# Kernel tuning notes

Hardware: AMD Instinct MI355X
Metric: run time of the kernel (lower is better)

## Reference

```python
import jax, jax.numpy as jnp
import numpy as np

N_EMBD = 1024
N_HEAD = 16
BLOCK_SIZE = 2048


def setup_inputs() -> dict:
    key = jax.random.key(0)
    k1, k2, k3 = jax.random.split(key, 3)
    B, T, C = 2, 2048, N_EMBD
    x = jax.random.normal(k1, (B, T, C), dtype=jnp.float32)
    # Dense(3*n_embd, use_bias=False): kernel [C, 3C]
    Wqkv = jax.random.normal(k2, (C, 3 * C), dtype=jnp.float32) * (1.0 / np.sqrt(C))
    # Output Dense(n_embd): kernel [C, C] + bias [C]
    Wout = jax.random.normal(k3, (C, C), dtype=jnp.float32) * (1.0 / np.sqrt(C))
    bout = jnp.zeros((C,), dtype=jnp.float32)
    return {"x": x, "Wqkv": Wqkv, "Wout": Wout, "bout": bout}


def reference(x, Wqkv, Wout, bout):
    B, T, C = x.shape
    H = N_HEAD
    hs = C // H  # head_size

    qkv = x @ Wqkv                       # [B, T, 3C]
    q, k, v = jnp.split(qkv, 3, axis=-1)  # each [B, T, C]
    q = q.reshape(B, T, H, hs).transpose(0, 2, 1, 3)  # [B, H, T, hs]
    k = k.reshape(B, T, H, hs).transpose(0, 2, 1, 3)
    v = v.reshape(B, T, H, hs).transpose(0, 2, 1, 3)

    att = jnp.einsum("bhqd,bhkd->bhqk", q, k) * (hs ** -0.5)  # [B, H, T, T]
    T_use = min(T, BLOCK_SIZE)
    mask = jnp.tril(jnp.ones((T_use, T_use), dtype=bool))
    att = jnp.where(mask, att, -jnp.inf)
    att = jax.nn.softmax(att, axis=-1)
    # dropout: deterministic (training=False) -> identity

    out = jnp.einsum("bhqk,bhkd->bhqd", att, v)  # [B, H, T, hs]
    out = out.transpose(0, 2, 1, 3).reshape(B, T, C)
    out = out @ Wout + bout
    return out
```

## Files before the change

kernel.cpp:

```cpp
#include <hip/hip_runtime.h>
#include <cstdint>
#include <cstddef>

#define BB 2
#define TT 2048
#define CC 1024
#define HH 16
#define HS 64
#define MM (BB*TT)
#define N1 (3*CC)

#define PST2 40

#define QSCALE 0.1803368801111243f

typedef __bf16 bf16_t;
typedef bf16_t bf16x8 __attribute__((ext_vector_type(8)));
typedef float  floatx4 __attribute__((ext_vector_type(4)));

__device__ __forceinline__ bf16_t f2bf(float f) {
    uint32_t u = __builtin_bit_cast(uint32_t, f);
    u += 0x7FFFu + ((u >> 16) & 1u);
    unsigned short s = (unsigned short)(u >> 16);
    return __builtin_bit_cast(bf16_t, s);
}

__device__ __forceinline__ void load_lds16(const bf16_t* g, bf16_t* l) {
    __builtin_amdgcn_global_load_lds((__attribute__((address_space(1))) void*)g,
                                     (__attribute__((address_space(3))) void*)l,
                                     16, 0, 0);
}

__device__ __forceinline__ void transpose_body(const float* __restrict__ src,
                                               bf16_t* __restrict__ dst,
                                               int R, int Ccol, int bx, int by,
                                               int tx, int ty, bf16_t (*tile)[33]) {
    int c0 = bx * 32, r0 = by * 32;
    for (int i = ty; i < 32; i += 8)
        tile[i][tx] = f2bf(src[(size_t)(r0 + i) * Ccol + c0 + tx]);
    __syncthreads();
    for (int i = ty; i < 32; i += 8)
        dst[(size_t)(c0 + i) * R + r0 + tx] = tile[tx][i];
}

__global__ __launch_bounds__(256) void k_prep(const float* __restrict__ x,
                                              const float* __restrict__ Wqkv,
                                              const float* __restrict__ Wout,
                                              bf16_t* __restrict__ xb,
                                              bf16_t* __restrict__ Wt1,
                                              bf16_t* __restrict__ Wt2) {
    __shared__ bf16_t tile[32][33];
    const int bid = blockIdx.x, tid = threadIdx.x;
    if (bid < 2048) {
        size_t i = ((size_t)bid * 256 + tid) * 8;
        float4 a = *(const float4*)(x + i);
        float4 b = *(const float4*)(x + i + 4);
        bf16x8 o;
        o[0] = f2bf(a.x); o[1] = f2bf(a.y); o[2] = f2bf(a.z); o[3] = f2bf(a.w);
        o[4] = f2bf(b.x); o[5] = f2bf(b.y); o[6] = f2bf(b.z); o[7] = f2bf(b.w);
        *(bf16x8*)(xb + i) = o;
    } else if (bid < 2048 + 3072) {
        int bb = bid - 2048;
        transpose_body(Wqkv, Wt1, CC, N1, bb % 96, bb / 96, tid & 31, tid >> 5, tile);
    } else {
        int bb = bid - 5120;
        transpose_body(Wout, Wt2, CC, CC, bb & 31, bb >> 5, tid & 31, tid >> 5, tile);
    }
}

__device__ __forceinline__ void gemm_core(const bf16_t* __restrict__ A,
                                          const bf16_t* __restrict__ Bt,
                                          bf16_t* As, bf16_t* Bs,
                                          int m0, int n0, int K,
                                          floatx4 acc[4][4]) {
    const int tid = threadIdx.x;
    const int wave = tid >> 6, lane = tid & 63;
    const int quad = lane >> 4, lrow = lane & 15;
    const int wm = wave >> 1, wn = wave & 1;
    const int lsub = lane >> 2;
    const int kc = lane & 3;

    for (int kk = 0; kk < K; kk += 32) {
        for (int s = 0; s < 2; ++s) {
            int rg = wave * 2 + s;
            const bf16_t* ga = A  + (size_t)(m0 + rg * 16 + lsub) * K + kk + kc * 8;
            const bf16_t* gb = Bt + (size_t)(n0 + rg * 16 + lsub) * K + kk + kc * 8;
            load_lds16(ga, As + rg * 512);
            load_lds16(gb, Bs + rg * 512);
        }
        __syncthreads();
        bf16x8 af[4], bfr[4];
        for (int i = 0; i < 4; ++i)
            af[i] = *(const bf16x8*)(As + (wm * 64 + i * 16 + lrow) * 32 + quad * 8);
        for (int j = 0; j < 4; ++j)
            bfr[j] = *(const bf16x8*)(Bs + (wn * 64 + j * 16 + lrow) * 32 + quad * 8);
        for (int i = 0; i < 4; ++i)
            for (int j = 0; j < 4; ++j)
                acc[i][j] = __builtin_amdgcn_mfma_f32_16x16x32_bf16(af[i], bfr[j], acc[i][j], 0, 0, 0);
        __syncthreads();
    }
}

__global__ __launch_bounds__(256, 2) void k_gemm_qkv(const bf16_t* __restrict__ x,
                                                     const bf16_t* __restrict__ Wt,
                                                     bf16_t* __restrict__ qb,
                                                     bf16_t* __restrict__ kb,
                                                     bf16_t* __restrict__ vt) {
    __shared__ bf16_t As[128 * 32];
    __shared__ bf16_t Bs[128 * 32];
    const int m0 = blockIdx.y * 128, n0 = blockIdx.x * 128;
    floatx4 acc[4][4];
    for (int i = 0; i < 4; ++i)
        for (int j = 0; j < 4; ++j)
            acc[i][j] = floatx4{0.f, 0.f, 0.f, 0.f};
    gemm_core(x, Wt, As, Bs, m0, n0, CC, acc);

    const int tid = threadIdx.x, wave = tid >> 6, lane = tid & 63;
    const int quad = lane >> 4, lrow = lane & 15;
    const int wm = wave >> 1, wn = wave & 1;
    const int b = m0 >> 11;
    for (int j = 0; j < 4; ++j) {
        int gn = n0 + wn * 64 + j * 16 + lrow;
        int which = gn >> 10, c = gn & 1023, h = c >> 6, d = c & 63;
        if (which == 0) {
            for (int i = 0; i < 4; ++i)
                for (int r = 0; r < 4; ++r) {
                    int t = (m0 & 2047) + wm * 64 + i * 16 + quad * 4 + r;
                    qb[((size_t)(b * HH + h) * TT + t) * HS + d] = f2bf(acc[i][j][r] * QSCALE);
                }
        } else if (which == 1) {
            for (int i = 0; i < 4; ++i)
                for (int r = 0; r < 4; ++r) {
                    int t = (m0 & 2047) + wm * 64 + i * 16 + quad * 4 + r;
                    kb[((size_t)(b * HH + h) * TT + t) * HS + d] = f2bf(acc[i][j][r]);
                }
        } else {
            for (int a = 0; a < 2; ++a) {
                bf16x8 pv;
                for (int r = 0; r < 4; ++r) {
                    pv[r * 2]     = f2bf(acc[2 * a][j][r]);
                    pv[r * 2 + 1] = f2bf(acc[2 * a + 1][j][r]);
                }
                int tb2 = (m0 & 2047) + wm * 64 + a * 32;
                *(bf16x8*)(vt + ((size_t)(b * HH + h) * HS + d) * TT + tb2 + quad * 8) = pv;
            }
        }
    }
}

__device__ static const signed char ORD[48][2] = {
    {15,-1},{31,0},{31,1},{30,0},{30,1},
    {14,-1},{29,0},{29,1},{28,0},{28,1},
    {13,-1},{27,0},{27,1},{26,0},{26,1},
    {12,-1},{25,0},{25,1},{24,0},{24,1},
    {11,-1},{23,0},{23,1},{22,0},{22,1},
    {10,-1},{21,0},{21,1},{20,0},{20,1},
    { 9,-1},{19,0},{19,1},{18,0},{18,1},
    { 8,-1},{17,0},{17,1},{16,0},{16,1},
    { 7,-1},{ 6,-1},{ 5,-1},{ 4,-1},{ 3,-1},{ 2,-1},{ 1,-1},{ 0,-1}
};

__global__ __launch_bounds__(128, 2) void k_attn(const bf16_t* __restrict__ qb,
                                                 const bf16_t* __restrict__ kb,
                                                 const bf16_t* __restrict__ vt,
                                                 bf16_t* __restrict__ yb,
                                                 float* __restrict__ o0,
                                                 float* __restrict__ o1,
                                                 float* __restrict__ l0,
                                                 float* __restrict__ l1) {
    __shared__ bf16_t Kb[2][32 * 72];
    __shared__ bf16_t Vb[2][64 * 40];
    __shared__ bf16_t Ps[2][2][32 * PST2];
    const int tid = threadIdx.x;
    const int w = tid >> 6, lane = tid & 63;
    const int quad = lane >> 4, lrow = lane & 15;
    const int bh = blockIdx.x & 31;
    const int j = blockIdx.x >> 5;
    const int qg = ORD[j][0];
    const int cc = ORD[j][1];
    const int ct = (cc < 0) ? (2 * qg + 2) : (qg + 1);
    const int key0 = (cc == 1) ? (qg + 1) * 32 : 0;
    const int kendl = 2 * qg + w + 1 - ((cc == 1) ? (qg + 1) : 0);
    const int kw = min(kendl, ct);
    const int q0 = qg * 64 + w * 32;

    const bf16_t* Qg = qb + (size_t)bh * TT * HS;
    const bf16_t* Kg = kb + (size_t)bh * TT * HS;
    const bf16_t* Vg = vt + (size_t)bh * HS * TT;

    const int skey = tid >> 2, scol = (tid & 3) * 16;
    const int svrow = tid >> 1, svcol = (tid & 1) * 16;

    bf16x8 kra, krb, vra, vrb;
    {
        const bf16_t* gk = Kg + (size_t)(key0 + skey) * HS + scol;
        kra = *(const bf16x8*)(gk);
        krb = *(const bf16x8*)(gk + 8);
        const bf16_t* gv = Vg + (size_t)svrow * TT + key0 + svcol;
        vra = *(const bf16x8*)(gv);
        vrb = *(const bf16x8*)(gv + 8);
        *(bf16x8*)(&Kb[0][skey * 72 + scol])     = kra;
        *(bf16x8*)(&Kb[0][skey * 72 + scol + 8]) = krb;
        *(bf16x8*)(&Vb[0][svrow * 40 + svcol])     = vra;
        *(bf16x8*)(&Vb[0][svrow * 40 + svcol + 8]) = vrb;
    }

    bf16x8 aq[2][2];
    for (int tq = 0; tq < 2; ++tq)
        for (int c = 0; c < 2; ++c)
            aq[tq][c] = *(const bf16x8*)(Qg + (size_t)(q0 + tq * 16 + lrow) * HS + c * 32 + quad * 8);

    const bf16_t onebf = __builtin_bit_cast(bf16_t, (unsigned short)0x3F80);
    bf16x8 bones = {onebf, onebf, onebf, onebf, onebf, onebf, onebf, onebf};

    floatx4 o[2][4];
    for (int tq = 0; tq < 2; ++tq)
        for (int dc = 0; dc < 4; ++dc) o[tq][dc] = floatx4{0.f, 0.f, 0.f, 0.f};
    floatx4 ol[2] = {floatx4{0.f,0.f,0.f,0.f}, floatx4{0.f,0.f,0.f,0.f}};

    bf16x8 bv_sav[4];
    const int wrow0 = quad * 4;

    for (int t = 0; t < ct; ++t) {
        __syncthreads();
        if (t + 1 < ct) {
            const bf16_t* gk = Kg + (size_t)(key0 + (t + 1) * 32 + skey) * HS + scol;
            kra = *(const bf16x8*)(gk);
            krb = *(const bf16x8*)(gk + 8);
            const bf16_t* gv = Vg + (size_t)svrow * TT + key0 + (t + 1) * 32 + svcol;
            vra = *(const bf16x8*)(gv);
            vrb = *(const bf16x8*)(gv + 8);
        }
        if (t < kw) {
            if (t > 0) {
                const bf16_t* Pp = &Ps[w][(t - 1) & 1][0];
                bf16x8 pa0 = *(const bf16x8*)(Pp + (size_t)lrow * PST2 + quad * 8);
                bf16x8 pa1 = *(const bf16x8*)(Pp + (size_t)(16 + lrow) * PST2 + quad * 8);
                o[0][0] = __builtin_amdgcn_mfma_f32_16x16x32_bf16(pa0, bv_sav[0], o[0][0], 0, 0, 0);
                o[0][1] = __builtin_amdgcn_mfma_f32_16x16x32_bf16(pa0, bv_sav[1], o[0][1], 0, 0, 0);
                o[0][2] = __builtin_amdgcn_mfma_f32_16x16x32_bf16(pa0, bv_sav[2], o[0][2], 0, 0, 0);
                o[0][3] = __builtin_amdgcn_mfma_f32_16x16x32_bf16(pa0, bv_sav[3], o[0][3], 0, 0, 0);
                ol[0]   = __builtin_amdgcn_mfma_f32_16x16x32_bf16(pa0, bones, ol[0], 0, 0, 0);
                o[1][0] = __builtin_amdgcn_mfma_f32_16x16x32_bf16(pa1, bv_sav[0], o[1][0], 0, 0, 0);
                o[1][1] = __builtin_amdgcn_mfma_f32_16x16x32_bf16(pa1, bv_sav[1], o[1][1], 0, 0, 0);
                o[1][2] = __builtin_amdgcn_mfma_f32_16x16x32_bf16(pa1, bv_sav[2], o[1][2], 0, 0, 0);
                o[1][3] = __builtin_amdgcn_mfma_f32_16x16x32_bf16(pa1, bv_sav[3], o[1][3], 0, 0, 0);
                ol[1]   = __builtin_amdgcn_mfma_f32_16x16x32_bf16(pa1, bones, ol[1], 0, 0, 0);
            }
            const bf16_t* Kt = &Kb[t & 1][0];
            const bf16_t* Vt = &Vb[t & 1][0];
            bf16x8 bk0 = *(const bf16x8*)(Kt + lrow * 72 + quad * 8);
            bf16x8 bk1 = *(const bf16x8*)(Kt + lrow * 72 + 32 + quad * 8);
            bf16x8 bk2 = *(const bf16x8*)(Kt + (16 + lrow) * 72 + quad * 8);
            bf16x8 bk3 = *(const bf16x8*)(Kt + (16 + lrow) * 72 + 32 + quad * 8);
            floatx4 s00 = floatx4{0.f,0.f,0.f,0.f}, s01 = s00, s10 = s00, s11 = s00;
            s00 = __builtin_amdgcn_mfma_f32_16x16x32_bf16(aq[0][0], bk0, s00, 0, 0, 0);
            s00 = __builtin_amdgcn_mfma_f32_16x16x32_bf16(aq[0][1], bk1, s00, 0, 0, 0);
            s01 = __builtin_amdgcn_mfma_f32_16x16x32_bf16(aq[0][0], bk2, s01, 0, 0, 0);
            s01 = __builtin_amdgcn_mfma_f32_16x16x32_bf16(aq[0][1], bk3, s01, 0, 0, 0);
            s10 = __builtin_amdgcn_mfma_f32_16x16x32_bf16(aq[1][0], bk0, s10, 0, 0, 0);
            s10 = __builtin_amdgcn_mfma_f32_16x16x32_bf16(aq[1][1], bk1, s10, 0, 0, 0);
            s11 = __builtin_amdgcn_mfma_f32_16x16x32_bf16(aq[1][0], bk2, s11, 0, 0, 0);
            s11 = __builtin_amdgcn_mfma_f32_16x16x32_bf16(aq[1][1], bk3, s11, 0, 0, 0);

            bv_sav[0] = *(const bf16x8*)(Vt + (0  + lrow) * 40 + quad * 8);
            bv_sav[1] = *(const bf16x8*)(Vt + (16 + lrow) * 40 + quad * 8);
            bv_sav[2] = *(const bf16x8*)(Vt + (32 + lrow) * 40 + quad * 8);
            bv_sav[3] = *(const bf16x8*)(Vt + (48 + lrow) * 40 + quad * 8);

            uint32_t* P32 = (uint32_t*)(&Ps[w][t & 1][0]);
            if (t < kendl - 1) {
                for (int r = 0; r < 4; ++r) {
                    float e00 = __builtin_amdgcn_exp2f(s00[r]);
                    float e01 = __builtin_amdgcn_exp2f(s01[r]);
                    float e10 = __builtin_amdgcn_exp2f(s10[r]);
                    float e11 = __builtin_amdgcn_exp2f(s11[r]);
                    uint32_t pk0 = __builtin_amdgcn_perm(
                        __builtin_bit_cast(uint32_t, e01),
                        __builtin_bit_cast(uint32_t, e00), 0x07060302u);
                    uint32_t pk1 = __builtin_amdgcn_perm(
                        __builtin_bit_cast(uint32_t, e11),
                        __builtin_bit_cast(uint32_t, e10), 0x07060302u);
                    P32[(wrow0 + r) * 20 + lrow]      = pk0;
                    P32[(wrow0 + r + 16) * 20 + lrow] = pk1;
                }
            } else {
                for (int r = 0; r < 4; ++r) {
                    bool keep = lrow <= quad * 4 + r;
                    float e00 = keep ? __builtin_amdgcn_exp2f(s00[r]) : 0.f;
                    float e01 = 0.f; (void)s01;
                    float e10 = __builtin_amdgcn_exp2f(s10[r]);
                    float e11 = keep ? __builtin_amdgcn_exp2f(s11[r]) : 0.f;
                    uint32_t pk0 = __builtin_amdgcn_perm(
                        __builtin_bit_cast(uint32_t, e01),
                        __builtin_bit_cast(uint32_t, e00), 0x07060302u);
                    uint32_t pk1 = __builtin_amdgcn_perm(
                        __builtin_bit_cast(uint32_t, e11),
                        __builtin_bit_cast(uint32_t, e10), 0x07060302u);
                    P32[(wrow0 + r) * 20 + lrow]      = pk0;
                    P32[(wrow0 + r + 16) * 20 + lrow] = pk1;
                }
            }
        }
        if (t + 1 < ct) {
            bf16_t* Kn = &Kb[(t + 1) & 1][0];
            bf16_t* Vn = &Vb[(t + 1) & 1][0];
            *(bf16x8*)(Kn + skey * 72 + scol)     = kra;
            *(bf16x8*)(Kn + skey * 72 + scol + 8) = krb;
            *(bf16x8*)(Vn + svrow * 40 + svcol)     = vra;
            *(bf16x8*)(Vn + svrow * 40 + svcol + 8) = vrb;
        }
    }

    asm volatile("s_waitcnt lgkmcnt(0)" ::: "memory");
    {
        const bf16_t* Pp = &Ps[w][(kw - 1) & 1][0];
        bf16x8 pa0 = *(const bf16x8*)(Pp + (size_t)lrow * PST2 + quad * 8);
        bf16x8 pa1 = *(const bf16x8*)(Pp + (size_t)(16 + lrow) * PST2 + quad * 8);
        o[0][0] = __builtin_amdgcn_mfma_f32_16x16x32_bf16(pa0, bv_sav[0], o[0][0], 0, 0, 0);
        o[0][1] = __builtin_amdgcn_mfma_f32_16x16x32_bf16(pa0, bv_sav[1], o[0][1], 0, 0, 0);
        o[0][2] = __builtin_amdgcn_mfma_f32_16x16x32_bf16(pa0, bv_sav[2], o[0][2], 0, 0, 0);
        o[0][3] = __builtin_amdgcn_mfma_f32_16x16x32_bf16(pa0, bv_sav[3], o[0][3], 0, 0, 0);
        ol[0]   = __builtin_amdgcn_mfma_f32_16x16x32_bf16(pa0, bones, ol[0], 0, 0, 0);
        o[1][0] = __builtin_amdgcn_mfma_f32_16x16x32_bf16(pa1, bv_sav[0], o[1][0], 0, 0, 0);
        o[1][1] = __builtin_amdgcn_mfma_f32_16x16x32_bf16(pa1, bv_sav[1], o[1][1], 0, 0, 0);
        o[1][2] = __builtin_amdgcn_mfma_f32_16x16x32_bf16(pa1, bv_sav[2], o[1][2], 0, 0, 0);
        o[1][3] = __builtin_amdgcn_mfma_f32_16x16x32_bf16(pa1, bv_sav[3], o[1][3], 0, 0, 0);
        ol[1]   = __builtin_amdgcn_mfma_f32_16x16x32_bf16(pa1, bones, ol[1], 0, 0, 0);
    }

    if (cc < 0) {
        const int b = bh >> 4, h = bh & 15;
        for (int tq = 0; tq < 2; ++tq)
            for (int r = 0; r < 4; ++r) {
                float inv = 1.0f / ol[tq][r];
                int q = q0 + tq * 16 + quad * 4 + r;
                for (int dc = 0; dc < 4; ++dc)
                    yb[(size_t)(b * TT + q) * CC + h * HS + dc * 16 + lrow] =
                        f2bf(o[tq][dc][r] * inv);
            }
    } else if (cc == 1) {
        for (int tq = 0; tq < 2; ++tq)
            for (int r = 0; r < 4; ++r) {
                int q = q0 + tq * 16 + quad * 4 + r;
                float* dst = o1 + ((size_t)(bh * 16 + qg - 16) * 64 + (q - qg * 64)) * 64 + lrow;
                for (int dc = 0; dc < 4; ++dc) dst[dc * 16] = o[tq][dc][r];
                if (lrow == 0) l1[(size_t)(bh * 16 + qg - 16) * 64 + (q - qg * 64)] = ol[tq][r];
            }
    } else {
        for (int tq = 0; tq < 2; ++tq)
            for (int r = 0; r < 4; ++r) {
                int q = q0 + tq * 16 + quad * 4 + r;
                float* dst = o0 + ((size_t)bh * TT + q) * HS + lrow;
                for (int dc = 0; dc < 4; ++dc) dst[dc * 16] = o[tq][dc][r];
                if (lrow == 0) l0[(size_t)bh * TT + q] = ol[tq][r];
            }
    }
}

__global__ __launch_bounds__(256) void k_norm(const float* __restrict__ o0,
                                              const float* __restrict__ o1,
                                              const float* __restrict__ l0,
                                              const float* __restrict__ l1,
                                              bf16_t* __restrict__ yb) {
    int idx = blockIdx.x * 256 + threadIdx.x;
    int d8 = idx & 7;
    int q  = 1024 + ((idx >> 3) & 1023);
    int bh = idx >> 13;
    int qg = q >> 6;
    const float* s0 = o0 + ((size_t)bh * TT + q) * HS + d8 * 8;
    const float* s1 = o1 + ((size_t)(bh * 16 + qg - 16) * 64 + (q & 63)) * 64 + d8 * 8;
    float4 a = *(const float4*)(s0);
    float4 b = *(const float4*)(s0 + 4);
    float4 a1 = *(const float4*)(s1);
    float4 b1 = *(const float4*)(s1 + 4);
    a.x += a1.x; a.y += a1.y; a.z += a1.z; a.w += a1.w;
    b.x += b1.x; b.y += b1.y; b.z += b1.z; b.w += b1.w;
    float l = l0[(size_t)bh * TT + q] + l1[(size_t)(bh * 16 + qg - 16) * 64 + (q & 63)];
    float inv = 1.0f / l;
    bf16x8 r;
    r[0] = f2bf(a.x * inv); r[1] = f2bf(a.y * inv);
    r[2] = f2bf(a.z * inv); r[3] = f2bf(a.w * inv);
    r[4] = f2bf(b.x * inv); r[5] = f2bf(b.y * inv);
    r[6] = f2bf(b.z * inv); r[7] = f2bf(b.w * inv);
    int bb = bh >> 4, h = bh & 15;
    *(bf16x8*)(yb + ((size_t)(bb * TT + q)) * CC + h * HS + d8 * 8) = r;
}

__global__ __launch_bounds__(256, 2) void k_gemm_out(const bf16_t* __restrict__ yin,
                                                     const bf16_t* __restrict__ Wt,
                                                     const float* __restrict__ bias,
                                                     float* __restrict__ out) {
    __shared__ bf16_t As[128 * 32];
    __shared__ bf16_t Bs[128 * 32];
    const int m0 = blockIdx.y * 128, n0 = blockIdx.x * 128;
    floatx4 acc[4][4];
    for (int i = 0; i < 4; ++i)
        for (int j = 0; j < 4; ++j)
            acc[i][j] = floatx4{0.f, 0.f, 0.f, 0.f};
    gemm_core(yin, Wt, As, Bs, m0, n0, CC, acc);

    const int tid = threadIdx.x, wave = tid >> 6, lane = tid & 63;
    const int quad = lane >> 4, lrow = lane & 15;
    const int wm = wave >> 1, wn = wave & 1;
    for (int i = 0; i < 4; ++i)
        for (int j = 0; j < 4; ++j) {
            int gn = n0 + wn * 64 + j * 16 + lrow;
            float bb = bias[gn];
            for (int r = 0; r < 4; ++r) {
                int gm = m0 + wm * 64 + i * 16 + quad * 4 + r;
                out[(size_t)gm * CC + gn] = acc[i][j][r] + bb;
            }
        }
}

extern "C" void kernel_launch(void* const* d_in, const int* in_sizes, int n_in,
                              void* d_out, int out_size, void* d_ws, size_t ws_size,
                              hipStream_t stream) {
    (void)in_sizes; (void)n_in; (void)out_size; (void)ws_size;
    const float* x    = (const float*)d_in[0];
    const float* Wqkv = (const float*)d_in[1];
    const float* Wout = (const float*)d_in[2];
    const float* bout = (const float*)d_in[3];
    float* out = (float*)d_out;

    bf16_t* xb  = (bf16_t*)d_ws;
    bf16_t* Wt1 = xb + (size_t)MM * CC;
    bf16_t* Wt2 = Wt1 + (size_t)N1 * CC;
    bf16_t* qb  = Wt2 + (size_t)CC * CC;
    bf16_t* kb  = qb + (size_t)BB * HH * TT * HS;
    bf16_t* vb  = kb + (size_t)BB * HH * TT * HS;
    bf16_t* yb  = vb + (size_t)BB * HH * TT * HS;
    float*  o0  = (float*)d_out;
    float*  o1  = (float*)xb;
    float*  l0  = (float*)Wt1;
    float*  l1  = l0 + (size_t)BB * HH * TT;

    k_prep<<<dim3(2048 + 3072 + 1024), 256, 0, stream>>>(x, Wqkv, Wout, xb, Wt1, Wt2);
    k_gemm_qkv<<<dim3(N1 / 128, MM / 128), 256, 0, stream>>>(xb, Wt1, qb, kb, vb);
    k_attn<<<dim3(48 * 32), 128, 0, stream>>>(qb, kb, vb, yb, o0, o1, l0, l1);
    k_norm<<<dim3(1024), 256, 0, stream>>>(o0, o1, l0, l1, yb);
    k_gemm_out<<<dim3(CC / 128, MM / 128), 256, 0, stream>>>(yb, Wt2, bout, out);
}
```

Before: 176.6 us.

## Rewrite QKV GEMM with 256x256 tiles, 4-stage LDS pipeline and XOR swizzle

The QKV projection GEMM now uses 256x256 output tiles per 512-thread block. Operands are staged through a 4-deep ring of LDS buffers, with global-to-LDS loads issued three K-steps ahead and gated by explicit vmcnt waits and barriers. LDS columns are XOR-swizzled to avoid bank conflicts, block IDs are remapped for L2 locality, and MFMA issue priority is raised with s_setprio. The aim is better operand reuse and hiding of memory latency, at the cost of heavier register/LDS use (128KB LDS) and only 192 blocks for the grid.

```diff
diff --git a/kernel.cpp b/kernel.cpp
--- a/kernel.cpp
+++ b/kernel.cpp
@@ -101,47 +101,117 @@
     }
 }
 
-__global__ __launch_bounds__(256, 2) void k_gemm_qkv(const bf16_t* __restrict__ x,
-                                                     const bf16_t* __restrict__ Wt,
-                                                     bf16_t* __restrict__ qb,
-                                                     bf16_t* __restrict__ kb,
-                                                     bf16_t* __restrict__ vt) {
-    __shared__ bf16_t As[128 * 32];
-    __shared__ bf16_t Bs[128 * 32];
-    const int m0 = blockIdx.y * 128, n0 = blockIdx.x * 128;
-    floatx4 acc[4][4];
-    for (int i = 0; i < 4; ++i)
-        for (int j = 0; j < 4; ++j)
-            acc[i][j] = floatx4{0.f, 0.f, 0.f, 0.f};
-    gemm_core(x, Wt, As, Bs, m0, n0, CC, acc);
-
-    const int tid = threadIdx.x, wave = tid >> 6, lane = tid & 63;
+__global__ __launch_bounds__(512) void k_gemm_qkv(const bf16_t* __restrict__ x,
+                                                  const bf16_t* __restrict__ Wt,
+                                                  bf16_t* __restrict__ qb,
+                                                  bf16_t* __restrict__ kb,
+                                                  bf16_t* __restrict__ vt) {
+    __shared__ bf16_t As[4][256 * 32];
+    __shared__ bf16_t Bs[4][256 * 32];
+    const int tid = threadIdx.x;
+    const int wave = tid >> 6, lane = tid & 63;
     const int quad = lane >> 4, lrow = lane & 15;
-    const int wm = wave >> 1, wn = wave & 1;
+    const int wm = wave >> 2, wn = wave & 3;
+
+    const int bid = blockIdx.y * 12 + blockIdx.x;
+    const int swz = (bid & 7) * 24 + (bid >> 3);
+    const int m0 = (swz / 12) * 256, n0 = (swz % 12) * 256;
+
+    floatx4 acc[8][4];
+    #pragma unroll
+    for (int i = 0; i < 8; ++i)
+        #pragma unroll
+        for (int j = 0; j < 4; ++j) acc[i][j] = floatx4{0.f, 0.f, 0.f, 0.f};
+
+    auto stage = [&](int kt) {
+        const int slot = kt & 3;
+        const int kk = kt * 32;
+        #pragma unroll
+        for (int l = 0; l < 2; ++l) {
+            int L = l * 512 + tid;
+            int row = L >> 2, cs = L & 3;
+            int gc = cs ^ ((row >> 1) & 3);
+            const bf16_t* ga = x  + (size_t)(m0 + row) * CC + kk + gc * 8;
+            const bf16_t* gb = Wt + (size_t)(n0 + row) * CC + kk + gc * 8;
+            load_lds16(ga, &As[slot][(size_t)(l * 512 + wave * 64) * 8]);
+            load_lds16(gb, &Bs[slot][(size_t)(l * 512 + wave * 64) * 8]);
+        }
+    };
+
+    auto do_tile = [&](int kt, bool st) {
+        const bf16_t* Ab = &As[kt & 3][0];
+        const bf16_t* Bb = &Bs[kt & 3][0];
+        const int csw = (quad ^ ((lrow >> 1) & 3)) * 8;
+        bf16x8 af[8], bfr[4];
+        #pragma unroll
+        for (int mf = 0; mf < 8; ++mf) {
+            int row = wm * 128 + mf * 16 + lrow;
+            af[mf] = *(const bf16x8*)(Ab + row * 32 + csw);
+        }
+        #pragma unroll
+        for (int nf = 0; nf < 4; ++nf) {
+            int row = wn * 64 + nf * 16 + lrow;
+            bfr[nf] = *(const bf16x8*)(Bb + row * 32 + csw);
+        }
+        if (st) stage(kt + 3);
+        __builtin_amdgcn_s_barrier();
+        __builtin_amdgcn_s_setprio(1);
+        #pragma unroll
+        for (int mf = 0; mf < 8; ++mf)
+            #pragma unroll
+            for (int nf = 0; nf < 4; ++nf)
+                acc[mf][nf] = __builtin_amdgcn_mfma_f32_16x16x32_bf16(af[mf], bfr[nf], acc[mf][nf], 0, 0, 0);
+        __builtin_amdgcn_s_setprio(0);
+    };
+
+    stage(0); stage(1); stage(2);
+    asm volatile("s_waitcnt vmcnt(8)" ::: "memory");
+    __builtin_amdgcn_s_barrier();
+
+    for (int kt = 0; kt < 29; ++kt) {
+        do_tile(kt, true);
+        asm volatile("s_waitcnt vmcnt(8)" ::: "memory");
+        __builtin_amdgcn_s_barrier();
+    }
+    do_tile(29, false);
+    asm volatile("s_waitcnt vmcnt(4)" ::: "memory");
+    __builtin_amdgcn_s_barrier();
+    do_tile(30, false);
+    asm volatile("s_waitcnt vmcnt(0)" ::: "memory");
+    __builtin_amdgcn_s_barrier();
+    do_tile(31, false);
+
     const int b = m0 >> 11;
-    for (int j = 0; j < 4; ++j) {
-        int gn = n0 + wn * 64 + j * 16 + lrow;
+    #pragma unroll
+    for (int nf = 0; nf < 4; ++nf) {
+        int gn = n0 + wn * 64 + nf * 16 + lrow;
         int which = gn >> 10, c = gn & 1023, h = c >> 6, d = c & 63;
         if (which == 0) {
-            for (int i = 0; i < 4; ++i)
+            #pragma unroll
+            for (int mf = 0; mf < 8; ++mf)
+                #pragma unroll
                 for (int r = 0; r < 4; ++r) {
-                    int t = (m0 & 2047) + wm * 64 + i * 16 + quad * 4 + r;
-                    qb[((size_t)(b * HH + h) * TT + t) * HS + d] = f2bf(acc[i][j][r] * QSCALE);
+                    int t = (m0 & 2047) + wm * 128 + mf * 16 + quad * 4 + r;
+                    qb[((size_t)(b * HH + h) * TT + t) * HS + d] = f2bf(acc[mf][nf][r] * QSCALE);
                 }
         } else if (which == 1) {
-            for (int i = 0; i < 4; ++i)
+            #pragma unroll
+            for (int mf = 0; mf < 8; ++mf)
+                #pragma unroll
                 for (int r = 0; r < 4; ++r) {
-                    int t = (m0 & 2047) + wm * 64 + i * 16 + quad * 4 + r;
-                    kb[((size_t)(b * HH + h) * TT + t) * HS + d] = f2bf(acc[i][j][r]);
+                    int t = (m0 & 2047) + wm * 128 + mf * 16 + quad * 4 + r;
+                    kb[((size_t)(b * HH + h) * TT + t) * HS + d] = f2bf(acc[mf][nf][r]);
                 }
         } else {
-            for (int a = 0; a < 2; ++a) {
+            #pragma unroll
+            for (int a = 0; a < 4; ++a) {
                 bf16x8 pv;
+                #pragma unroll
                 for (int r = 0; r < 4; ++r) {
-                    pv[r * 2]     = f2bf(acc[2 * a][j][r]);
-                    pv[r * 2 + 1] = f2bf(acc[2 * a + 1][j][r]);
+                    pv[r * 2]     = f2bf(acc[2 * a][nf][r]);
+                    pv[r * 2 + 1] = f2bf(acc[2 * a + 1][nf][r]);
                 }
-                int tb2 = (m0 & 2047) + wm * 64 + a * 32;
+                int tb2 = (m0 & 2047) + wm * 128 + a * 32;
                 *(bf16x8*)(vt + ((size_t)(b * HH + h) * HS + d) * TT + tb2 + quad * 8) = pv;
             }
         }
@@ -437,7 +507,7 @@
     float*  l1  = l0 + (size_t)BB * HH * TT;
 
     k_prep<<<dim3(2048 + 3072 + 1024), 256, 0, stream>>>(x, Wqkv, Wout, xb, Wt1, Wt2);
-    k_gemm_qkv<<<dim3(N1 / 128, MM / 128), 256, 0, stream>>>(xb, Wt1, qb, kb, vb);
+    k_gemm_qkv<<<dim3(N1 / 256, MM / 256), 512, 0, stream>>>(xb, Wt1, qb, kb, vb);
     k_attn<<<dim3(48 * 32), 128, 0, stream>>>(qb, kb, vb, yb, o0, o1, l0, l1);
     k_norm<<<dim3(1024), 256, 0, stream>>>(o0, o1, l0, l1, yb);
     k_gemm_out<<<dim3(CC / 128, MM / 128), 256, 0, stream>>>(yb, Wt2, bout, out);
```

Result: slower. 180.2 us (+2.1%).
